# Kernel optimization log

Hardware: AMD Instinct MI355X
Metric: run time of the kernel (lower is better)

## Reference

```python
import jax, jax.numpy as jnp
import numpy as np

N_HEADS = 16

def setup_inputs() -> dict:
    key = jax.random.key(0)
    k0, k1, k2 = jax.random.split(key, 3)
    B, T, C = 4, 2048, 1024
    x = jax.random.normal(k0, (B, T, C), dtype=jnp.float32)
    # nn.Linear params: y = x @ W.T + b
    w_qkv = jax.random.normal(k1, (3 * C, C), dtype=jnp.float32) * 0.02
    b_qkv = jnp.zeros((3 * C,), dtype=jnp.float32)
    w_proj = jax.random.normal(k2, (C, C), dtype=jnp.float32) * 0.02
    b_proj = jnp.zeros((C,), dtype=jnp.float32)
    return {"x": x, "w_qkv": w_qkv, "b_qkv": b_qkv, "w_proj": w_proj, "b_proj": b_proj}

def reference(x, w_qkv, b_qkv, w_proj, b_proj):
    B, T, C = x.shape
    H = N_HEADS
    hd = C // H
    qkv = x @ w_qkv.T + b_qkv                      # [B, T, 3C]
    q, k, v = jnp.split(qkv, 3, axis=-1)           # each [B, T, C]
    q = q.reshape(B, T, H, hd).transpose(0, 2, 1, 3)  # [B, H, T, hd]
    k = k.reshape(B, T, H, hd).transpose(0, 2, 1, 3)
    v = v.reshape(B, T, H, hd).transpose(0, 2, 1, 3)
    # note: original scales by emb_dim**-0.5 (C), not head_dim**-0.5
    wei = jnp.einsum("bhqd,bhkd->bhqk", q, k) * (C ** -0.5)  # [B, H, T, T]
    causal = jnp.tril(jnp.ones((T, T), dtype=bool))
    wei = jnp.where(causal, wei, -jnp.inf)
    att = jax.nn.softmax(wei, axis=-1)
    out = jnp.einsum("bhqk,bhkd->bhqd", att, v)    # [B, H, T, hd]
    out = out.transpose(0, 2, 1, 3).reshape(B, T, C)
    return out @ w_proj.T + b_proj
```

## Files before the change

### kernel.cpp

```cpp
#include <hip/hip_runtime.h>
#include <hip/hip_bf16.h>

typedef __bf16 bf16;
typedef __bf16 bf16x8 __attribute__((ext_vector_type(8)));
typedef __bf16 bf16x4 __attribute__((ext_vector_type(4)));
typedef float  f32x4  __attribute__((ext_vector_type(4)));
typedef short  short4_t __attribute__((ext_vector_type(4)));

#define LDS_ASYNC16(g, l)                                            \
  __builtin_amdgcn_global_load_lds(                                  \
      (const __attribute__((address_space(1))) void*)(g),            \
      (__attribute__((address_space(3))) void*)(l), 16, 0, 0)

#define QSCALE 0.04508421995f

__global__ void cvt3_f32_bf16(const float* __restrict__ i0, bf16* __restrict__ o0, int n0,
                              const float* __restrict__ i1, bf16* __restrict__ o1, int n1,
                              const float* __restrict__ i2, bf16* __restrict__ o2, int n2) {
  int i = blockIdx.x * blockDim.x + threadIdx.x;
  const float* in;
  bf16* out;
  if (i < n0) {
    in = i0; out = o0;
  } else if (i < n0 + n1) {
    i -= n0; in = i1; out = o1;
  } else {
    i -= n0 + n1;
    if (i >= n2) return;
    in = i2; out = o2;
  }
  float4 v = ((const float4*)in)[i];
  bf16x4 o = {(bf16)v.x, (bf16)v.y, (bf16)v.z, (bf16)v.w};
  ((bf16x4*)out)[i] = o;
}

template <int MODE>
__global__ __launch_bounds__(256) void gemm_bt(
    const bf16* __restrict__ A, const bf16* __restrict__ B,
    const float* __restrict__ bias, float* __restrict__ outf,
    bf16* __restrict__ oq, bf16* __restrict__ ok, bf16* __restrict__ ov,
    int M, int N, int K) {
  __shared__ bf16 As[2][128 * 32];
  __shared__ bf16 Bs[2][128 * 32];
  const int tid = threadIdx.x;
  const int wave = tid >> 6, lane = tid & 63;
  const int quad = lane >> 4, l15 = lane & 15;
  const int bm = blockIdx.x * 128, bn = blockIdx.y * 128;
  const int wrow = (wave >> 1) << 6, wcol = (wave & 1) << 6;
  const int srow = tid >> 2;
  const int schunk = (tid & 3) * 8;

  f32x4 acc[4][4] = {};

  const bf16* ga0 = A + (size_t)(bm + srow) * K + schunk;
  const bf16* ga1 = A + (size_t)(bm + srow + 64) * K + schunk;
  const bf16* gb0 = B + (size_t)(bn + srow) * K + schunk;
  const bf16* gb1 = B + (size_t)(bn + srow + 64) * K + schunk;
  char* lA = (char*)As + wave * 1024;
  char* lB = (char*)Bs + wave * 1024;

  for (int k0 = 0; k0 < K; k0 += 64) {
    __syncthreads();
    LDS_ASYNC16(ga0 + k0, lA);
    LDS_ASYNC16(ga1 + k0, lA + 4096);
    LDS_ASYNC16(gb0 + k0, lB);
    LDS_ASYNC16(gb1 + k0, lB + 4096);
    LDS_ASYNC16(ga0 + k0 + 32, lA + 8192);
    LDS_ASYNC16(ga1 + k0 + 32, lA + 8192 + 4096);
    LDS_ASYNC16(gb0 + k0 + 32, lB + 8192);
    LDS_ASYNC16(gb1 + k0 + 32, lB + 8192 + 4096);
    __syncthreads();
#pragma unroll
    for (int s = 0; s < 2; ++s) {
      bf16x8 af[4], bfr[4];
#pragma unroll
      for (int mi = 0; mi < 4; ++mi)
        af[mi] = *(const bf16x8*)&As[s][(wrow + mi * 16 + l15) * 32 + quad * 8];
#pragma unroll
      for (int ni = 0; ni < 4; ++ni)
        bfr[ni] = *(const bf16x8*)&Bs[s][(wcol + ni * 16 + l15) * 32 + quad * 8];
#pragma unroll
      for (int mi = 0; mi < 4; ++mi)
#pragma unroll
        for (int ni = 0; ni < 4; ++ni)
          acc[mi][ni] = __builtin_amdgcn_mfma_f32_16x16x32_bf16(
              af[mi], bfr[ni], acc[mi][ni], 0, 0, 0);
    }
  }

#pragma unroll
  for (int mi = 0; mi < 4; ++mi) {
    const int row0 = bm + wrow + mi * 16 + quad * 4;
#pragma unroll
    for (int ni = 0; ni < 4; ++ni) {
      const int col = bn + wcol + ni * 16 + l15;
      const float bv = bias[col];
      if (MODE == 0) {
#pragma unroll
        for (int r = 0; r < 4; ++r)
          outf[(size_t)(row0 + r) * N + col] = acc[mi][ni][r] + bv;
      } else {
        const int part = col >> 10;
        const int cn = col & 1023, h = cn >> 6, d = cn & 63;
        const int b = row0 >> 11, t0 = row0 & 2047;
        if (part == 2) {
          bf16x4 pk = {(bf16)(acc[mi][ni][0] + bv), (bf16)(acc[mi][ni][1] + bv),
                       (bf16)(acc[mi][ni][2] + bv), (bf16)(acc[mi][ni][3] + bv)};
          *(bf16x4*)(ov + ((size_t)(b * 16 + h) * 64 + d) * 2048 + t0) = pk;
        } else {
          const float sc = part ? 1.0f : QSCALE;
          bf16* dst = (part ? ok : oq) + ((size_t)(b * 16 + h) * 2048 + t0) * 64 + d;
#pragma unroll
          for (int r = 0; r < 4; ++r)
            dst[(size_t)r * 64] = (bf16)((acc[mi][ni][r] + bv) * sc);
        }
      }
    }
  }
}

__global__ __launch_bounds__(256) void flash_attn(
    const bf16* __restrict__ qb, const bf16* __restrict__ kb,
    const bf16* __restrict__ vt, bf16* __restrict__ ob) {
  constexpr int T = 2048;
  __shared__ bf16 Ks[2][64 * 72];
  __shared__ bf16 Vs[2][64 * 72];
  __shared__ float Ls[4][2][4][16];
  const int tid = threadIdx.x, wave = tid >> 6, lane = tid & 63;
  const int quad = lane >> 4, l15 = lane & 15;
  const int bh = blockIdx.x;
  const int b = bh >> 4, h = bh & 15;
  const bf16* qbase = qb + (size_t)bh * T * 64;
  const bf16* kbase = kb + (size_t)bh * T * 64;
  const bf16* vbase = vt + (size_t)bh * 64 * T;
  const int srow = tid >> 3, sc = (tid & 7) * 8;

  const int qt = 15 - (int)blockIdx.y;
  const int q0 = qt * 128 + wave * 32;

  bf16x8 qf[2][2];
#pragma unroll
  for (int qi = 0; qi < 2; ++qi)
#pragma unroll
    for (int ks = 0; ks < 2; ++ks)
      qf[qi][ks] = *(const bf16x8*)(qbase + (size_t)(q0 + qi * 16 + l15) * 64 +
                                    ks * 32 + quad * 8);

  f32x4 lsumv[2] = {};
  f32x4 oacc[2][4] = {};

  const int nkt = 2 * qt + 2;
  const int ktp = q0 >> 6;

  {
    uint4 k0 = *(const uint4*)(kbase + (size_t)srow * 64 + sc);
    uint4 k1 = *(const uint4*)(kbase + (size_t)(srow + 32) * 64 + sc);
    uint4 v0 = *(const uint4*)(vbase + (size_t)srow * T + sc);
    uint4 v1 = *(const uint4*)(vbase + (size_t)(srow + 32) * T + sc);
    *(uint4*)&Ks[0][srow * 72 + sc] = k0;
    *(uint4*)&Ks[0][(srow + 32) * 72 + sc] = k1;
    *(uint4*)&Vs[0][srow * 72 + sc] = v0;
    *(uint4*)&Vs[0][(srow + 32) * 72 + sc] = v1;
  }

#pragma unroll 1
  for (int kt = 0; kt < nkt; ++kt) {
    __syncthreads();
    const int cur = kt & 1;
    const bool pre = (kt + 1) < nkt;
    uint4 pk0, pk1, pv0, pv1;
    if (pre) {
      const bf16* kp = kbase + (size_t)(kt + 1) * 64 * 64;
      const bf16* vp = vbase + (kt + 1) * 64;
      pk0 = *(const uint4*)(kp + (size_t)srow * 64 + sc);
      pk1 = *(const uint4*)(kp + (size_t)(srow + 32) * 64 + sc);
      pv0 = *(const uint4*)(vp + (size_t)srow * T + sc);
      pv1 = *(const uint4*)(vp + (size_t)(srow + 32) * T + sc);
    }
    if (kt <= ktp) {
      f32x4 st[4][2];
#pragma unroll
      for (int ki = 0; ki < 4; ++ki) {
        bf16x8 kfa = *(const bf16x8*)&Ks[cur][(ki * 16 + l15) * 72 + quad * 8];
        bf16x8 kfb =
            *(const bf16x8*)&Ks[cur][(ki * 16 + l15) * 72 + 32 + quad * 8];
#pragma unroll
        for (int qi = 0; qi < 2; ++qi) {
          f32x4 a = {0.f, 0.f, 0.f, 0.f};
          a = __builtin_amdgcn_mfma_f32_16x16x32_bf16(kfa, qf[qi][0], a, 0, 0, 0);
          a = __builtin_amdgcn_mfma_f32_16x16x32_bf16(kfb, qf[qi][1], a, 0, 0, 0);
          st[ki][qi] = a;
        }
      }
      if (kt == ktp) {
#pragma unroll
        for (int ki = 0; ki < 4; ++ki)
#pragma unroll
          for (int qi = 0; qi < 2; ++qi)
#pragma unroll
            for (int r = 0; r < 4; ++r) {
              const int kcol = kt * 64 + ki * 16 + quad * 4 + r;
              const int qrow = q0 + qi * 16 + l15;
              if (kcol > qrow) st[ki][qi][r] = -__builtin_inff();
            }
      }
      short4_t pa[4][2];
#pragma unroll
      for (int ki = 0; ki < 4; ++ki)
#pragma unroll
        for (int qi = 0; qi < 2; ++qi) {
#pragma unroll
          for (int r = 0; r < 4; ++r)
            st[ki][qi][r] = __builtin_amdgcn_exp2f(st[ki][qi][r]);
          lsumv[qi] += st[ki][qi];
          bf16x4 pk = {(bf16)st[ki][qi][0], (bf16)st[ki][qi][1],
                       (bf16)st[ki][qi][2], (bf16)st[ki][qi][3]};
          pa[ki][qi] = __builtin_bit_cast(short4_t, pk);
        }
#pragma unroll
      for (int di = 0; di < 4; ++di)
#pragma unroll
        for (int ki = 0; ki < 4; ++ki) {
          bf16x4 vv = *(const bf16x4*)&Vs[cur][(di * 16 + l15) * 72 + ki * 16 +
                                              quad * 4];
          short4_t vb = __builtin_bit_cast(short4_t, vv);
#pragma unroll
          for (int qi = 0; qi < 2; ++qi)
            oacc[qi][di] = __builtin_amdgcn_mfma_f32_16x16x16bf16_1k(
                pa[ki][qi], vb, oacc[qi][di], 0, 0, 0);
        }
    }
    if (pre) {
      const int nxt = cur ^ 1;
      *(uint4*)&Ks[nxt][srow * 72 + sc] = pk0;
      *(uint4*)&Ks[nxt][(srow + 32) * 72 + sc] = pk1;
      *(uint4*)&Vs[nxt][srow * 72 + sc] = pv0;
      *(uint4*)&Vs[nxt][(srow + 32) * 72 + sc] = pv1;
    }
  }

#pragma unroll
  for (int qi = 0; qi < 2; ++qi)
    Ls[wave][qi][quad][l15] =
        lsumv[qi][0] + lsumv[qi][1] + lsumv[qi][2] + lsumv[qi][3];
#pragma unroll
  for (int qi = 0; qi < 2; ++qi)
#pragma unroll
    for (int r = 0; r < 4; ++r) {
      const int rloc = quad * 4 + r;
      const float l = Ls[wave][qi][0][rloc] + Ls[wave][qi][1][rloc] +
                      Ls[wave][qi][2][rloc] + Ls[wave][qi][3][rloc];
      const float inv = 1.f / l;
      const int t = q0 + qi * 16 + rloc;
#pragma unroll
      for (int di = 0; di < 4; ++di) {
        const int d = di * 16 + l15;
        ob[((size_t)b * 2048 + t) * 1024 + h * 64 + d] =
            (bf16)(oacc[qi][di][r] * inv);
      }
    }
}

extern "C" void kernel_launch(void* const* d_in, const int* in_sizes, int n_in,
                              void* d_out, int out_size, void* d_ws,
                              size_t ws_size, hipStream_t stream) {
  const float* x = (const float*)d_in[0];
  const float* w_qkv = (const float*)d_in[1];
  const float* b_qkv = (const float*)d_in[2];
  const float* w_proj = (const float*)d_in[3];
  const float* b_proj = (const float*)d_in[4];
  float* out = (float*)d_out;

  const int B = 4, T = 2048, C = 1024;
  const size_t nx = (size_t)B * T * C;

  char* ws = (char*)d_ws;
  bf16* xb = (bf16*)ws;      ws += nx * 2;
  bf16* wqkvb = (bf16*)ws;   ws += (size_t)3 * C * C * 2;
  bf16* wprojb = (bf16*)ws;  ws += (size_t)C * C * 2;
  bf16* qb = (bf16*)ws;      ws += nx * 2;
  bf16* kbuf = (bf16*)ws;    ws += nx * 2;
  bf16* vtb = (bf16*)ws;     ws += nx * 2;
  bf16* attb = (bf16*)ws;    ws += nx * 2;

  const int n0 = (int)(nx / 4), n1 = 3 * C * C / 4, n2 = C * C / 4;
  cvt3_f32_bf16<<<(n0 + n1 + n2 + 255) / 256, 256, 0, stream>>>(
      x, xb, n0, w_qkv, wqkvb, n1, w_proj, wprojb, n2);

  dim3 g1(64, 24);
  gemm_bt<1><<<g1, 256, 0, stream>>>(xb, wqkvb, b_qkv, nullptr, qb, kbuf, vtb,
                                     B * T, 3 * C, C);
  dim3 g2(64, 16);
  flash_attn<<<g2, 256, 0, stream>>>(qb, kbuf, vtb, attb);

  dim3 g3(64, 8);
  gemm_bt<0><<<g3, 256, 0, stream>>>(attb, wprojb, b_proj, out, nullptr,
                                     nullptr, nullptr, B * T, C, C);
}
```

Measured before the change: 251.2 us.

## Use 16x16x32 MFMA for PV product with permuted V tile layout

The P·V product now uses the 16x16x32 bf16 MFMA instead of the 16x16x16 variant, halving the number of MFMA issues and V fragment loads per tile. To make this work, the V tile columns are permuted when stored to LDS so each lane's 8-element fragment matches the P layout built from two adjacent key sub-tiles. It also wraps the MFMA blocks in s_setprio to favour matrix issue over other waves. The store to LDS becomes split 8-byte writes, which may add bank conflicts or store instructions.

```diff
diff --git a/kernel.cpp b/kernel.cpp
--- a/kernel.cpp
+++ b/kernel.cpp
@@ -5,7 +5,6 @@
 typedef __bf16 bf16x8 __attribute__((ext_vector_type(8)));
 typedef __bf16 bf16x4 __attribute__((ext_vector_type(4)));
 typedef float  f32x4  __attribute__((ext_vector_type(4)));
-typedef short  short4_t __attribute__((ext_vector_type(4)));
 
 #define LDS_ASYNC16(g, l)                                            \
   __builtin_amdgcn_global_load_lds(                                  \
@@ -135,6 +134,8 @@
   const bf16* vbase = vt + (size_t)bh * 64 * T;
   const int srow = tid >> 3, sc = (tid & 7) * 8;
 
+  const int vp0 = (sc & ~31) | ((sc & 8) << 1) | ((sc & 16) >> 2);
+
   const int qt = 15 - (int)blockIdx.y;
   const int q0 = qt * 128 + wave * 32;
 
@@ -159,8 +160,10 @@
     uint4 v1 = *(const uint4*)(vbase + (size_t)(srow + 32) * T + sc);
     *(uint4*)&Ks[0][srow * 72 + sc] = k0;
     *(uint4*)&Ks[0][(srow + 32) * 72 + sc] = k1;
-    *(uint4*)&Vs[0][srow * 72 + sc] = v0;
-    *(uint4*)&Vs[0][(srow + 32) * 72 + sc] = v1;
+    *(uint2*)&Vs[0][srow * 72 + vp0] = make_uint2(v0.x, v0.y);
+    *(uint2*)&Vs[0][srow * 72 + vp0 + 8] = make_uint2(v0.z, v0.w);
+    *(uint2*)&Vs[0][(srow + 32) * 72 + vp0] = make_uint2(v1.x, v1.y);
+    *(uint2*)&Vs[0][(srow + 32) * 72 + vp0 + 8] = make_uint2(v1.z, v1.w);
   }
 
 #pragma unroll 1
@@ -179,6 +182,7 @@
     }
     if (kt <= ktp) {
       f32x4 st[4][2];
+      __builtin_amdgcn_s_setprio(1);
 #pragma unroll
       for (int ki = 0; ki < 4; ++ki) {
         bf16x8 kfa = *(const bf16x8*)&Ks[cur][(ki * 16 + l15) * 72 + quad * 8];
@@ -192,6 +196,7 @@
           st[ki][qi] = a;
         }
       }
+      __builtin_amdgcn_s_setprio(0);
       if (kt == ktp) {
 #pragma unroll
         for (int ki = 0; ki < 4; ++ki)
@@ -204,7 +209,6 @@
               if (kcol > qrow) st[ki][qi][r] = -__builtin_inff();
             }
       }
-      short4_t pa[4][2];
 #pragma unroll
       for (int ki = 0; ki < 4; ++ki)
 #pragma unroll
@@ -213,29 +217,42 @@
           for (int r = 0; r < 4; ++r)
             st[ki][qi][r] = __builtin_amdgcn_exp2f(st[ki][qi][r]);
           lsumv[qi] += st[ki][qi];
-          bf16x4 pk = {(bf16)st[ki][qi][0], (bf16)st[ki][qi][1],
-                       (bf16)st[ki][qi][2], (bf16)st[ki][qi][3]};
-          pa[ki][qi] = __builtin_bit_cast(short4_t, pk);
-        }
+        }
+      bf16x8 pa8[2][2];
+#pragma unroll
+      for (int ki2 = 0; ki2 < 2; ++ki2)
+#pragma unroll
+        for (int qi = 0; qi < 2; ++qi) {
+          bf16x8 p;
+#pragma unroll
+          for (int r = 0; r < 4; ++r) {
+            p[r] = (bf16)st[2 * ki2][qi][r];
+            p[r + 4] = (bf16)st[2 * ki2 + 1][qi][r];
+          }
+          pa8[ki2][qi] = p;
+        }
+      __builtin_amdgcn_s_setprio(1);
 #pragma unroll
       for (int di = 0; di < 4; ++di)
 #pragma unroll
-        for (int ki = 0; ki < 4; ++ki) {
-          bf16x4 vv = *(const bf16x4*)&Vs[cur][(di * 16 + l15) * 72 + ki * 16 +
-                                              quad * 4];
-          short4_t vb = __builtin_bit_cast(short4_t, vv);
+        for (int ki2 = 0; ki2 < 2; ++ki2) {
+          bf16x8 vv = *(const bf16x8*)&Vs[cur][(di * 16 + l15) * 72 + ki2 * 32 +
+                                              quad * 8];
 #pragma unroll
           for (int qi = 0; qi < 2; ++qi)
-            oacc[qi][di] = __builtin_amdgcn_mfma_f32_16x16x16bf16_1k(
-                pa[ki][qi], vb, oacc[qi][di], 0, 0, 0);
-        }
+            oacc[qi][di] = __builtin_amdgcn_mfma_f32_16x16x32_bf16(
+                pa8[ki2][qi], vv, oacc[qi][di], 0, 0, 0);
+        }
+      __builtin_amdgcn_s_setprio(0);
     }
     if (pre) {
       const int nxt = cur ^ 1;
       *(uint4*)&Ks[nxt][srow * 72 + sc] = pk0;
       *(uint4*)&Ks[nxt][(srow + 32) * 72 + sc] = pk1;
-      *(uint4*)&Vs[nxt][srow * 72 + sc] = pv0;
-      *(uint4*)&Vs[nxt][(srow + 32) * 72 + sc] = pv1;
+      *(uint2*)&Vs[nxt][srow * 72 + vp0] = make_uint2(pv0.x, pv0.y);
+      *(uint2*)&Vs[nxt][srow * 72 + vp0 + 8] = make_uint2(pv0.z, pv0.w);
+      *(uint2*)&Vs[nxt][(srow + 32) * 72 + vp0] = make_uint2(pv1.x, pv1.y);
+      *(uint2*)&Vs[nxt][(srow + 32) * 72 + vp0 + 8] = make_uint2(pv1.z, pv1.w);
     }
   }
 
```

Result: faster. 239.9 us (-4.5%).
